# Kernel optimization log

Hardware: AMD Instinct MI355X
Metric: run time of the kernel (lower is better)

Reference implementation:

```python
import jax, jax.numpy as jnp
import numpy as np


def setup_inputs() -> dict:
    key = jax.random.key(0)
    k1, k2, k3, k4, k5 = jax.random.split(key, 5)
    B, L, H = 32, 2048, 768
    in1 = jax.random.normal(k1, (B, H), dtype=jnp.float32)
    in2 = jax.random.normal(k2, (B, H), dtype=jnp.float32)
    text = jax.random.normal(k3, (B, L, H), dtype=jnp.float32)
    textmask = jnp.ones((B, L), dtype=jnp.float32)  # 1 = valid token
    # learned params (nn.Linear weights are [out, in]); small scale avoids tanh saturation
    W2 = jax.random.normal(k4, (H, 3 * H), dtype=jnp.float32) * 0.02
    b2 = jnp.zeros((H,), dtype=jnp.float32)
    W1 = jax.random.normal(k5, (1, H), dtype=jnp.float32) * 0.02
    b1 = jnp.zeros((1,), dtype=jnp.float32)
    return {"in1": in1, "in2": in2, "text": text, "textmask": textmask,
            "W2": W2, "b2": b2, "W1": W1, "b1": b1}


def reference(in1, in2, text, textmask, W2, b2, W1, b1):
    H = in1.shape[-1]
    # Split linear2 weight along input dim instead of materializing cat([in1,in2,text]).
    # Same math: cat @ W2.T == in1@W2a.T + in2@W2b.T + text@W2c.T
    W2a, W2b, W2c = W2[:, :H], W2[:, H:2 * H], W2[:, 2 * H:]
    bias_bh = in1 @ W2a.T + in2 @ W2b.T + b2          # [B, H], broadcast over L
    h = jnp.tanh(jnp.einsum('blh,gh->blg', text, W2c) + bias_bh[:, None, :])  # [B, L, H]
    att = jnp.einsum('blh,h->bl', h, W1[0]) + b1[0]   # [B, L]
    att = jax.nn.softmax((1.0 - textmask) * (-1e20) + att, axis=-1)  # masked softmax [B, L]
    context = jnp.einsum('bl,blh->bh', att, text)     # weighted sum [B, H]
    return context, att[:, None, :]                   # matches (context, att[B,1,L])
```

## Files before the change

kernel.cpp:

```cpp
#include <hip/hip_runtime.h>
#include <hip/hip_bf16.h>

typedef __bf16 bf16x8 __attribute__((ext_vector_type(8)));
typedef __bf16 bf16x4 __attribute__((ext_vector_type(4)));
typedef float  f32x4  __attribute__((ext_vector_type(4)));

#define H 768
#define LSEQ 2048
#define BATCH 32
#define MROWS (BATCH*LSEQ)
#define NT 3
#define W2S 2304

__device__ __forceinline__ void gload_lds16(const void* g, void* l){
  __builtin_amdgcn_global_load_lds((const __attribute__((address_space(1))) void*)g,
                                   (__attribute__((address_space(3))) void*)l, 16, 0, 0);
}

__global__ void w2c_cvt_k(const float* __restrict__ W2, __bf16* __restrict__ w2cb){
  int i4 = blockIdx.x*256 + threadIdx.x;
  int g  = i4 / 192;
  int hc = (i4 % 192) * 4;
  f32x4 v = *(const f32x4*)(W2 + (size_t)g*W2S + 1536 + hc);
  bf16x4 o; o[0]=(__bf16)v[0]; o[1]=(__bf16)v[1]; o[2]=(__bf16)v[2]; o[3]=(__bf16)v[3];
  *(bf16x4*)(w2cb + (size_t)g*H + hc) = o;
}

__global__ void bias_k(const float* __restrict__ in1, const float* __restrict__ in2,
                       const float* __restrict__ W2, const float* __restrict__ b2,
                       float* __restrict__ bias){
  int b = blockIdx.y;
  int g = blockIdx.x*64 + (threadIdx.x & 63);
  int q = threadIdx.x >> 6;
  const float* wa = W2 + (size_t)g*W2S + q*192;
  const float* wb = wa + H;
  const float* x1 = in1 + b*H + q*192;
  const float* x2 = in2 + b*H + q*192;
  float acc = 0.f;
  #pragma unroll 8
  for (int h=0; h<192; h+=4){
    f32x4 a4 = *(const f32x4*)(wa+h);
    f32x4 c4 = *(const f32x4*)(x1+h);
    f32x4 b4 = *(const f32x4*)(wb+h);
    f32x4 d4 = *(const f32x4*)(x2+h);
    acc += a4[0]*c4[0]+a4[1]*c4[1]+a4[2]*c4[2]+a4[3]*c4[3];
    acc += b4[0]*d4[0]+b4[1]*d4[1]+b4[2]*d4[2]+b4[3]*d4[3];
  }
  __shared__ float sm[4][64];
  sm[q][threadIdx.x&63] = acc;
  __syncthreads();
  if (q==0){
    float r = sm[0][threadIdx.x]+sm[1][threadIdx.x]+sm[2][threadIdx.x]+sm[3][threadIdx.x] + b2[g];
    bias[(size_t)b*H + g] = r;
  }
}

__global__ __launch_bounds__(256,2) void fused_gemm_att_k(
    const float* __restrict__ text, const __bf16* __restrict__ w2cb,
    const float* __restrict__ bias, const float* __restrict__ W1,
    float* __restrict__ attp)
{
  __shared__ __align__(16) __bf16 a_lds[2][128*32];
  __shared__ __align__(16) __bf16 b_lds[2][256*32];
  __shared__ float att_lds[2][128];

  int lin = blockIdx.x;
  int mt  = lin / 3;
  int nt  = lin % 3;
  int b   = mt >> 4;
  int m0  = mt << 7;
  int t = threadIdx.x, lane = t & 63, wid = t >> 6;
  int wm = wid >> 1, wn = wid & 1;

  const float*  atile = text + (size_t)m0*H;
  const __bf16* btile = w2cb + (size_t)(nt*256)*H;

  f32x4 acc[4][8];
  #pragma unroll
  for (int mi=0;mi<4;++mi)
    #pragma unroll
    for (int ni=0;ni<8;++ni) acc[mi][ni] = (f32x4){0.f,0.f,0.f,0.f};

  int ar = t>>3, ac = (t&7)*4;
  f32x4 aReg[4];

  auto loadA = [&](int kk){
    #pragma unroll
    for (int j=0;j<4;++j)
      aReg[j] = *(const f32x4*)(atile + (size_t)(ar + j*32)*H + kk*32 + ac);
  };
  auto writeA = [&](int bf){
    #pragma unroll
    for (int j=0;j<4;++j){
      bf16x4 o; o[0]=(__bf16)aReg[j][0]; o[1]=(__bf16)aReg[j][1];
                o[2]=(__bf16)aReg[j][2]; o[3]=(__bf16)aReg[j][3];
      *(bf16x4*)&a_lds[bf][(ar + j*32)*32 + ac] = o;
    }
  };
  auto stageB = [&](int bf, int kk){
    #pragma unroll
    for (int j=0;j<4;++j){
      int slot = wid*4 + j;
      int n  = slot*16 + (lane>>2);
      gload_lds16(btile + (size_t)n*H + kk*32 + (lane&3)*8, &b_lds[bf][slot*512]);
    }
  };
  auto compute = [&](int bf){
    bf16x8 af[4];
    int kq = (lane>>4)*8;
    #pragma unroll
    for (int mi=0;mi<4;++mi)
      af[mi] = *(const bf16x8*)&a_lds[bf][(wm*64 + mi*16 + (lane&15))*32 + kq];
    #pragma unroll
    for (int ni=0;ni<8;++ni){
      bf16x8 bq = *(const bf16x8*)&b_lds[bf][(wn*128 + ni*16 + (lane&15))*32 + kq];
      #pragma unroll
      for (int mi=0;mi<4;++mi)
        acc[mi][ni] = __builtin_amdgcn_mfma_f32_16x16x32_bf16(af[mi], bq, acc[mi][ni], 0,0,0);
    }
  };

  loadA(0);
  writeA(0);
  stageB(0, 0);
  loadA(1);
  __syncthreads();

  #pragma unroll 2
  for (int kk=0; kk<24; ++kk){
    int nxt = (kk+1)&1;
    if (kk+1 < 24){
      stageB(nxt, kk+1);
      writeA(nxt);
      if (kk+2 < 24) loadA(kk+2);
    }
    compute(kk&1);
    __syncthreads();
  }

  float bb[8], ww[8];
  int gb = nt*256 + wn*128 + (lane&15);
  #pragma unroll
  for (int ni=0;ni<8;++ni){ bb[ni]=bias[(size_t)b*H + gb + ni*16]; ww[ni]=W1[gb + ni*16]; }

  float av[16];
  #pragma unroll
  for (int mi=0;mi<4;++mi)
    #pragma unroll
    for (int r=0;r<4;++r){
      float s = 0.f;
      #pragma unroll
      for (int ni=0;ni<8;++ni){
        float x = acc[mi][ni][r] + bb[ni];
        float e = __expf(2.0f*x);
        s += ww[ni] * ((e-1.0f)/(e+1.0f));
      }
      av[mi*4+r] = s;
    }
  #pragma unroll
  for (int off=1; off<16; off<<=1)
    #pragma unroll
    for (int i=0;i<16;++i) av[i] += __shfl_xor(av[i], off);

  if ((lane&15)==0){
    int mg = (lane>>4)*4;
    #pragma unroll
    for (int mi=0;mi<4;++mi)
      #pragma unroll
      for (int r=0;r<4;++r)
        att_lds[wn][wm*64 + mi*16 + mg + r] = av[mi*4+r];
  }
  __syncthreads();
  if (t < 128) attp[(size_t)nt*MROWS + m0 + t] = att_lds[0][t] + att_lds[1][t];
}

__global__ void softmax_k(const float* __restrict__ attp, const float* __restrict__ tmask,
                          const float* __restrict__ b1, float* __restrict__ att){
  int b = blockIdx.x, t = threadIdx.x;
  int lane = t & 63, wv = t >> 6;
  __shared__ float sl[LSEQ];
  __shared__ float red[4];
  float b1v = b1[0];
  float lmax = -3.0e38f;
  for (int i=t; i<LSEQ; i+=256){
    float v = b1v;
    #pragma unroll
    for (int p=0;p<NT;++p) v += attp[(size_t)p*MROWS + b*LSEQ + i];
    v += (1.0f - tmask[b*LSEQ+i]) * -1.0e20f;
    sl[i] = v;
    lmax = fmaxf(lmax, v);
  }
  #pragma unroll
  for (int off=32; off>=1; off>>=1) lmax = fmaxf(lmax, __shfl_xor(lmax, off));
  if (lane==0) red[wv] = lmax;
  __syncthreads();
  float mx = fmaxf(fmaxf(red[0],red[1]), fmaxf(red[2],red[3]));
  __syncthreads();
  float lsum = 0.f;
  for (int i=t; i<LSEQ; i+=256){
    float e = __expf(sl[i]-mx);
    sl[i] = e;
    lsum += e;
  }
  #pragma unroll
  for (int off=32; off>=1; off>>=1) lsum += __shfl_xor(lsum, off);
  if (lane==0) red[wv] = lsum;
  __syncthreads();
  float inv = 1.0f/(red[0]+red[1]+red[2]+red[3]);
  for (int i=t; i<LSEQ; i+=256) att[(size_t)b*LSEQ+i] = sl[i]*inv;
}

__global__ void ctxpart_k(const float* __restrict__ text, const float* __restrict__ att,
                          float* __restrict__ ctxp){
  int chunk = blockIdx.x, b = blockIdx.y, t = threadIdx.x;
  const float* tp = text + ((size_t)(b*LSEQ + chunk*64))*H + 4*t;
  const float* ap = att + (size_t)b*LSEQ + chunk*64;
  f32x4 acc = {0.f,0.f,0.f,0.f};
  #pragma unroll 4
  for (int l=0;l<64;++l){
    float a = ap[l];
    f32x4 v = *(const f32x4*)(tp + (size_t)l*H);
    acc[0] += a*v[0]; acc[1] += a*v[1]; acc[2] += a*v[2]; acc[3] += a*v[3];
  }
  *(f32x4*)(ctxp + ((size_t)(b*32+chunk))*H + 4*t) = acc;
}

__global__ void ctxred_k(const float* __restrict__ ctxp, float* __restrict__ out){
  int b = blockIdx.x, h = threadIdx.x;
  float s = 0.f;
  #pragma unroll 8
  for (int c=0;c<32;++c) s += ctxp[((size_t)(b*32+c))*H + h];
  out[(size_t)b*H + h] = s;
}

extern "C" void kernel_launch(void* const* d_in, const int* in_sizes, int n_in,
                              void* d_out, int out_size, void* d_ws, size_t ws_size,
                              hipStream_t stream){
  (void)in_sizes; (void)n_in; (void)out_size; (void)ws_size;
  const float* in1   = (const float*)d_in[0];
  const float* in2   = (const float*)d_in[1];
  const float* text  = (const float*)d_in[2];
  const float* tmask = (const float*)d_in[3];
  const float* W2    = (const float*)d_in[4];
  const float* b2    = (const float*)d_in[5];
  const float* W1    = (const float*)d_in[6];
  const float* b1    = (const float*)d_in[7];
  float* out = (float*)d_out;
  char*  ws  = (char*)d_ws;
  __bf16* w2cb = (__bf16*)(ws);
  float* biasb = (float*)(ws + 1179648);
  float* attp  = (float*)(ws + 1277952);
  float* ctxp  = (float*)(ws + 2850816);
  float* att_out = out + BATCH*H;

  w2c_cvt_k      <<<dim3(576),   dim3(256), 0, stream>>>(W2, w2cb);
  bias_k         <<<dim3(12,32), dim3(256), 0, stream>>>(in1, in2, W2, b2, biasb);
  fused_gemm_att_k<<<dim3(1536), dim3(256), 0, stream>>>(text, w2cb, biasb, W1, attp);
  softmax_k      <<<dim3(32),    dim3(256), 0, stream>>>(attp, tmask, b1, att_out);
  ctxpart_k      <<<dim3(32,32), dim3(192), 0, stream>>>(text, att_out, ctxp);
  ctxred_k       <<<dim3(32),    dim3(768), 0, stream>>>(ctxp, out);
}
```

Baseline: 198.3 us.

## Restructure fused GEMM to 256x256 tiles with 8 waves, swizzled LDS and interleaved pipeline

The fused GEMM+attention kernel now uses 512-thread blocks computing 256x256 tiles, which halves how often each text row is re-read across N tiles per block count. The main loop is split into four MFMA phases with explicit barriers, priority bumps and interleaved global loads, LDS writes and LDS reads. LDS rows are XOR-swizzled to cut bank conflicts, block IDs are remapped for locality, and the tanh divide is replaced by a fast reciprocal. The cost is higher register pressure and more complex synchronisation, which could limit occupancy.

```diff
diff --git a/kernel.cpp b/kernel.cpp
--- a/kernel.cpp
+++ b/kernel.cpp
@@ -16,6 +16,11 @@
   __builtin_amdgcn_global_load_lds((const __attribute__((address_space(1))) void*)g,
                                    (__attribute__((address_space(3))) void*)l, 16, 0, 0);
 }
+
+#define PBAR() do{ __builtin_amdgcn_sched_barrier(0); __builtin_amdgcn_s_barrier(); \
+  asm volatile("s_waitcnt lgkmcnt(0)" ::: "memory"); __builtin_amdgcn_sched_barrier(0);}while(0)
+#define CBAR() do{ __builtin_amdgcn_sched_barrier(0); __builtin_amdgcn_s_barrier(); \
+  __builtin_amdgcn_sched_barrier(0);}while(0)
 
 __global__ void w2c_cvt_k(const float* __restrict__ W2, __bf16* __restrict__ w2cb){
   int i4 = blockIdx.x*256 + threadIdx.x;
@@ -55,123 +60,149 @@
   }
 }
 
-__global__ __launch_bounds__(256,2) void fused_gemm_att_k(
+__global__ __launch_bounds__(512,2) void fused_gemm_att_k(
     const float* __restrict__ text, const __bf16* __restrict__ w2cb,
     const float* __restrict__ bias, const float* __restrict__ W1,
     float* __restrict__ attp)
 {
-  __shared__ __align__(16) __bf16 a_lds[2][128*32];
+  __shared__ __align__(16) __bf16 a_lds[2][256*32];
   __shared__ __align__(16) __bf16 b_lds[2][256*32];
-  __shared__ float att_lds[2][128];
-
-  int lin = blockIdx.x;
+  __shared__ float att_lds[4][256];
+
+  int bid = blockIdx.x;
+  int lin = (bid & 7)*96 + (bid >> 3);
   int mt  = lin / 3;
   int nt  = lin % 3;
-  int b   = mt >> 4;
-  int m0  = mt << 7;
+  int m0  = mt << 8;
+  int b   = m0 >> 11;
   int t = threadIdx.x, lane = t & 63, wid = t >> 6;
-  int wm = wid >> 1, wn = wid & 1;
+  int wm = wid >> 2, wn = wid & 3;
 
   const float*  atile = text + (size_t)m0*H;
   const __bf16* btile = w2cb + (size_t)(nt*256)*H;
 
-  f32x4 acc[4][8];
-  #pragma unroll
-  for (int mi=0;mi<4;++mi)
-    #pragma unroll
-    for (int ni=0;ni<8;++ni) acc[mi][ni] = (f32x4){0.f,0.f,0.f,0.f};
-
-  int ar = t>>3, ac = (t&7)*4;
+  f32x4 acc[8][4];
+  #pragma unroll
+  for (int mi=0;mi<8;++mi)
+    #pragma unroll
+    for (int ni=0;ni<4;++ni) acc[mi][ni] = (f32x4){0.f,0.f,0.f,0.f};
+
+  int arow = t>>1, acg = t&1;
+  const float* aptr = atile + (size_t)arow*H + acg*16;
+  int aswz = (arow>>1)&3;
+  int aw0 = arow*32 + (((2*acg  )^aswz)*8);
+  int aw1 = arow*32 + (((2*acg+1)^aswz)*8);
   f32x4 aReg[4];
 
+  int slot0 = wid*2, slot1 = wid*2+1;
+  int bn0 = slot0*16 + (lane>>2), bn1 = slot1*16 + (lane>>2);
+  const __bf16* bsrc0 = btile + (size_t)bn0*H + (((lane&3)^((bn0>>1)&3))*8);
+  const __bf16* bsrc1 = btile + (size_t)bn1*H + (((lane&3)^((bn1>>1)&3))*8);
+
   auto loadA = [&](int kk){
     #pragma unroll
-    for (int j=0;j<4;++j)
-      aReg[j] = *(const f32x4*)(atile + (size_t)(ar + j*32)*H + kk*32 + ac);
+    for (int j=0;j<4;++j) aReg[j] = *(const f32x4*)(aptr + kk*32 + j*4);
   };
   auto writeA = [&](int bf){
-    #pragma unroll
-    for (int j=0;j<4;++j){
-      bf16x4 o; o[0]=(__bf16)aReg[j][0]; o[1]=(__bf16)aReg[j][1];
-                o[2]=(__bf16)aReg[j][2]; o[3]=(__bf16)aReg[j][3];
-      *(bf16x4*)&a_lds[bf][(ar + j*32)*32 + ac] = o;
+    bf16x8 lo, hi;
+    lo[0]=(__bf16)aReg[0][0]; lo[1]=(__bf16)aReg[0][1]; lo[2]=(__bf16)aReg[0][2]; lo[3]=(__bf16)aReg[0][3];
+    lo[4]=(__bf16)aReg[1][0]; lo[5]=(__bf16)aReg[1][1]; lo[6]=(__bf16)aReg[1][2]; lo[7]=(__bf16)aReg[1][3];
+    hi[0]=(__bf16)aReg[2][0]; hi[1]=(__bf16)aReg[2][1]; hi[2]=(__bf16)aReg[2][2]; hi[3]=(__bf16)aReg[2][3];
+    hi[4]=(__bf16)aReg[3][0]; hi[5]=(__bf16)aReg[3][1]; hi[6]=(__bf16)aReg[3][2]; hi[7]=(__bf16)aReg[3][3];
+    *(bf16x8*)&a_lds[bf][aw0] = lo;
+    *(bf16x8*)&a_lds[bf][aw1] = hi;
+  };
+  auto stageB = [&](int bf, int kk){
+    gload_lds16(bsrc0 + kk*32, &b_lds[bf][slot0*512]);
+    gload_lds16(bsrc1 + kk*32, &b_lds[bf][slot1*512]);
+  };
+
+  int fr = lane&15, fc = lane>>4;
+  auto rdA = [&](int bf, int mh, bf16x8* af){
+    #pragma unroll
+    for (int mi=0;mi<4;++mi){
+      int row = wm*128 + mh*64 + mi*16 + fr;
+      af[mi] = *(const bf16x8*)&a_lds[bf][row*32 + ((fc^((row>>1)&3))*8)];
     }
   };
-  auto stageB = [&](int bf, int kk){
-    #pragma unroll
-    for (int j=0;j<4;++j){
-      int slot = wid*4 + j;
-      int n  = slot*16 + (lane>>2);
-      gload_lds16(btile + (size_t)n*H + kk*32 + (lane&3)*8, &b_lds[bf][slot*512]);
+  auto rdB = [&](int bf, int nh, bf16x8* bq){
+    #pragma unroll
+    for (int j=0;j<2;++j){
+      int n = wn*64 + nh*32 + j*16 + fr;
+      bq[j] = *(const bf16x8*)&b_lds[bf][n*32 + ((fc^((n>>1)&3))*8)];
     }
   };
-  auto compute = [&](int bf){
-    bf16x8 af[4];
-    int kq = (lane>>4)*8;
+  auto mfma8 = [&](int mh, int nh, bf16x8* af, bf16x8* bq){
+    __builtin_amdgcn_s_setprio(1);
     #pragma unroll
     for (int mi=0;mi<4;++mi)
-      af[mi] = *(const bf16x8*)&a_lds[bf][(wm*64 + mi*16 + (lane&15))*32 + kq];
-    #pragma unroll
-    for (int ni=0;ni<8;++ni){
-      bf16x8 bq = *(const bf16x8*)&b_lds[bf][(wn*128 + ni*16 + (lane&15))*32 + kq];
       #pragma unroll
-      for (int mi=0;mi<4;++mi)
-        acc[mi][ni] = __builtin_amdgcn_mfma_f32_16x16x32_bf16(af[mi], bq, acc[mi][ni], 0,0,0);
-    }
+      for (int j=0;j<2;++j)
+        acc[mh*4+mi][nh*2+j] =
+          __builtin_amdgcn_mfma_f32_16x16x32_bf16(af[mi], bq[j], acc[mh*4+mi][nh*2+j], 0,0,0);
+    __builtin_amdgcn_s_setprio(0);
   };
 
   loadA(0);
+  stageB(0, 0);
   writeA(0);
-  stageB(0, 0);
-  loadA(1);
-  __syncthreads();
+  asm volatile("s_waitcnt vmcnt(0) lgkmcnt(0)" ::: "memory");
+  __builtin_amdgcn_s_barrier();
 
   #pragma unroll 2
-  for (int kk=0; kk<24; ++kk){
-    int nxt = (kk+1)&1;
-    if (kk+1 < 24){
-      stageB(nxt, kk+1);
-      writeA(nxt);
-      if (kk+2 < 24) loadA(kk+2);
-    }
-    compute(kk&1);
-    __syncthreads();
-  }
-
-  float bb[8], ww[8];
-  int gb = nt*256 + wn*128 + (lane&15);
-  #pragma unroll
-  for (int ni=0;ni<8;++ni){ bb[ni]=bias[(size_t)b*H + gb + ni*16]; ww[ni]=W1[gb + ni*16]; }
-
-  float av[16];
-  #pragma unroll
-  for (int mi=0;mi<4;++mi)
+  for (int s=0; s<24; ++s){
+    int p = s&1, q = p^1;
+    bf16x8 a0[4], a1[4], b0[2], b1[2];
+    rdA(p,0,a0); rdB(p,0,b0);
+    if (s<23) loadA(s+1);
+    PBAR(); mfma8(0,0,a0,b0); CBAR();
+    rdB(p,1,b1);
+    if (s<23) stageB(q, s+1);
+    PBAR(); mfma8(0,1,a0,b1); CBAR();
+    rdA(p,1,a1);
+    if (s<23) writeA(q);
+    PBAR(); mfma8(1,1,a1,b1); CBAR();
+    rdB(p,0,b0);
+    PBAR(); mfma8(1,0,a1,b0);
+    if (s<23) asm volatile("s_waitcnt vmcnt(0)" ::: "memory");
+    CBAR();
+  }
+
+  float bb[4], ww[4];
+  int gb = nt*256 + wn*64 + fr;
+  #pragma unroll
+  for (int ni=0;ni<4;++ni){ bb[ni]=bias[(size_t)b*H + gb + ni*16]; ww[ni]=W1[gb + ni*16]; }
+
+  float av[32];
+  #pragma unroll
+  for (int mi=0;mi<8;++mi)
     #pragma unroll
     for (int r=0;r<4;++r){
       float s = 0.f;
       #pragma unroll
-      for (int ni=0;ni<8;++ni){
+      for (int ni=0;ni<4;++ni){
         float x = acc[mi][ni][r] + bb[ni];
         float e = __expf(2.0f*x);
-        s += ww[ni] * ((e-1.0f)/(e+1.0f));
+        s += ww[ni] * ((e-1.0f)*__builtin_amdgcn_rcpf(e+1.0f));
       }
       av[mi*4+r] = s;
     }
   #pragma unroll
   for (int off=1; off<16; off<<=1)
     #pragma unroll
-    for (int i=0;i<16;++i) av[i] += __shfl_xor(av[i], off);
-
-  if ((lane&15)==0){
-    int mg = (lane>>4)*4;
-    #pragma unroll
-    for (int mi=0;mi<4;++mi)
+    for (int i=0;i<32;++i) av[i] += __shfl_xor(av[i], off);
+
+  if (fr==0){
+    #pragma unroll
+    for (int mi=0;mi<8;++mi)
       #pragma unroll
       for (int r=0;r<4;++r)
-        att_lds[wn][wm*64 + mi*16 + mg + r] = av[mi*4+r];
-  }
-  __syncthreads();
-  if (t < 128) attp[(size_t)nt*MROWS + m0 + t] = att_lds[0][t] + att_lds[1][t];
+        att_lds[wn][wm*128 + mi*16 + fc*4 + r] = av[mi*4+r];
+  }
+  __syncthreads();
+  if (t < 256)
+    attp[(size_t)nt*MROWS + m0 + t] =
+      att_lds[0][t] + att_lds[1][t] + att_lds[2][t] + att_lds[3][t];
 }
 
 __global__ void softmax_k(const float* __restrict__ attp, const float* __restrict__ tmask,
@@ -255,7 +286,7 @@
 
   w2c_cvt_k      <<<dim3(576),   dim3(256), 0, stream>>>(W2, w2cb);
   bias_k         <<<dim3(12,32), dim3(256), 0, stream>>>(in1, in2, W2, b2, biasb);
-  fused_gemm_att_k<<<dim3(1536), dim3(256), 0, stream>>>(text, w2cb, biasb, W1, attp);
+  fused_gemm_att_k<<<dim3(768),  dim3(512), 0, stream>>>(text, w2cb, biasb, W1, attp);
   softmax_k      <<<dim3(32),    dim3(256), 0, stream>>>(attp, tmask, b1, att_out);
   ctxpart_k      <<<dim3(32,32), dim3(192), 0, stream>>>(text, att_out, ctxp);
   ctxred_k       <<<dim3(32),    dim3(768), 0, stream>>>(ctxp, out);
```

Result: slower. 206.7 us (+4.2%).
